# Optimization experiments

Hardware: AMD Instinct MI355X
Metric: run time of the kernel (lower is better)

Reference implementation:

```python
import jax, jax.numpy as jnp
import numpy as np

K_BUCKET = 144  # bucket size k from __init__


def setup_inputs() -> dict:
    key = jax.random.key(0)
    k1, k2 = jax.random.split(key)
    B, C, H, W = 8, 256, 96, 96
    A = 4                      # n_attentions (hash rounds)
    m = min((H * W) // 144, 128)  # = 64, per the source's m formula
    inputs = jax.random.normal(k1, (B, C, H, W), dtype=jnp.float32)
    random_matrices = jax.random.normal(k2, (A, C, m), dtype=jnp.float32)
    return {"inputs": inputs, "random_matrices": random_matrices}


def reference(inputs, random_matrices):
    B, C, H, W = inputs.shape
    A = random_matrices.shape[0]
    S = H * W
    k = K_BUCKET
    nb = S // k  # number of buckets

    # flatten(2,3).permute(0,2,1): [B, S, C]
    xf = inputs.reshape(B, C, S).transpose(0, 2, 1)

    # LSH random projection: [B, A, S, m]
    rot = jnp.einsum('bsc,acm->basm', xf, random_matrices)
    # max-hash over projection dim: [B, A, S]
    hash_code = jnp.max(rot, axis=-1)

    # descending sort -> permutation of sequence positions per (batch, round)
    idx = jnp.argsort(-hash_code, axis=2)            # [B, A, S] int

    # gather features into hash order: [B, A, S, C]
    xg = jnp.take_along_axis(xf[:, None, :, :], idx[..., None], axis=2)
    # split into buckets of size k: [B, A, nb, k, C]
    xb = xg.reshape(B, A, nb, k, C)

    # per-bucket self-attention (non-local attention restricted to bucket)
    scale = 1.0 / jnp.sqrt(jnp.asarray(C, dtype=xb.dtype))
    scores = jnp.einsum('banic,banjc->banij', xb, xb) * scale  # [B,A,nb,k,k]
    probs = jax.nn.softmax(scores, axis=-1)
    ob = jnp.einsum('banij,banjc->banic', probs, xb)           # [B,A,nb,k,C]

    # scatter bucket outputs back to original positions via inverse permutation
    out_sorted = ob.reshape(B, A, S, C)
    inv = jnp.argsort(idx, axis=2)                             # inverse permutation
    out = jnp.take_along_axis(out_sorted, inv[..., None], axis=2)  # [B,A,S,C]

    # average over hash rounds -> [B, S, C] (output layout matches torch.zeros(n,h*w,c))
    return jnp.mean(out, axis=1)
```

## Files before the change

kernel.cpp:

```cpp
#include <hip/hip_runtime.h>
#include <math.h>

#define B_ 8
#define C_ 256
#define S_ 9216
#define A_ 4
#define K_ 144
#define NB_ 64
#define SORTN 16384
#define XSS 261

typedef __bf16 bf16x8 __attribute__((ext_vector_type(8)));
typedef float f32x4 __attribute__((ext_vector_type(4)));
typedef double f64x4 __attribute__((ext_vector_type(4)));
#define MFMA(a, b, c) __builtin_amdgcn_mfma_f32_16x16x32_bf16(a, b, c, 0, 0, 0)
#define MFMA64(a, b, c) __builtin_amdgcn_mfma_f64_16x16x4f64(a, b, c, 0, 0, 0)

__device__ __forceinline__ unsigned short f2bf(float f) {
  unsigned int u = __float_as_uint(f);
  u = (u + 0x7FFFu + ((u >> 16) & 1u)) >> 16;
  return (unsigned short)u;
}
__device__ __forceinline__ float bf2f(unsigned short u) {
  return __uint_as_float(((unsigned int)u) << 16);
}

__global__ __launch_bounds__(256) void t_kernel(const float* __restrict__ in,
                                                unsigned short* __restrict__ xf16) {
  __shared__ float tile[32][33];
  int b = blockIdx.z;
  int c0 = blockIdx.y << 5, s0 = blockIdx.x << 5;
  int x = threadIdx.x & 31, y = threadIdx.x >> 5;
  const float* ip = in + ((size_t)b * C_ + c0 + y) * S_ + s0 + x;
#pragma unroll
  for (int k = 0; k < 32; k += 8) tile[y + k][x] = ip[(size_t)k * S_];
  __syncthreads();
  int xx = threadIdx.x & 15;
  int yy = threadIdx.x >> 4;
#pragma unroll
  for (int k = 0; k < 32; k += 16) {
    int s = s0 + yy + k;
    unsigned int* dst = (unsigned int*)(xf16 + ((size_t)b * S_ + s) * C_ + c0);
    dst[xx] = (unsigned int)f2bf(tile[2 * xx][yy + k]) |
              ((unsigned int)f2bf(tile[2 * xx + 1][yy + k]) << 16);
  }
}

__global__ __launch_bounds__(256) void cvt_r_kernel(const float* __restrict__ RM,
                                                    double* __restrict__ R64) {
  int i = blockIdx.x * 256 + threadIdx.x;
  if (i < A_ * C_ * 64) R64[i] = (double)RM[i];
}

__global__ __launch_bounds__(256, 2) void hash_kernel(const float* __restrict__ in,
                                                      const double* __restrict__ R64,
                                                      unsigned long long* __restrict__ keys) {
  __shared__ float Xs[64 * XSS];
  int blk = blockIdx.x;
  int chunk = blk % (S_ / 64);
  int b = blk / (S_ / 64);
  int s0 = chunk * 64;
  int tid = threadIdx.x;
  int a = __builtin_amdgcn_readfirstlane(tid >> 6);
  int lane = tid & 63, lr = lane & 15, lg = lane >> 4;

  for (int e = tid; e < C_ * 16; e += 256) {
    int c = e >> 4, sq = (e & 15) << 2;
    float4 v = *(const float4*)&in[((size_t)b * C_ + c) * S_ + s0 + sq];
    Xs[(sq + 0) * XSS + c] = v.x;
    Xs[(sq + 1) * XSS + c] = v.y;
    Xs[(sq + 2) * XSS + c] = v.z;
    Xs[(sq + 3) * XSS + c] = v.w;
  }
  __syncthreads();

  const double* __restrict__ Rb = R64 + (size_t)a * C_ * 64;
  f64x4 acc[4][4];
#pragma unroll
  for (int rt = 0; rt < 4; ++rt)
#pragma unroll
    for (int ct = 0; ct < 4; ++ct) acc[rt][ct] = (f64x4){0.0, 0.0, 0.0, 0.0};

#pragma unroll 2
  for (int k = 0; k < 64; ++k) {
    int c = k * 4 + lg;
    double bv[4], av[4];
#pragma unroll
    for (int ct = 0; ct < 4; ++ct) bv[ct] = Rb[(size_t)c * 64 + ct * 16 + lr];
#pragma unroll
    for (int rt = 0; rt < 4; ++rt) av[rt] = (double)Xs[(rt * 16 + lr) * XSS + c];
#pragma unroll
    for (int rt = 0; rt < 4; ++rt)
#pragma unroll
      for (int ct = 0; ct < 4; ++ct) acc[rt][ct] = MFMA64(av[rt], bv[ct], acc[rt][ct]);
  }

  unsigned long long* kb = keys + ((size_t)(b * A_ + a)) * SORTN;
#pragma unroll
  for (int rt = 0; rt < 4; ++rt) {
    double mj[4];
#pragma unroll
    for (int j = 0; j < 4; ++j) {
      double m0 = acc[rt][0][j] > acc[rt][1][j] ? acc[rt][0][j] : acc[rt][1][j];
      double m1 = acc[rt][2][j] > acc[rt][3][j] ? acc[rt][2][j] : acc[rt][3][j];
      mj[j] = m0 > m1 ? m0 : m1;
    }
#pragma unroll
    for (int off = 1; off < 16; off <<= 1)
#pragma unroll
      for (int j = 0; j < 4; ++j) {
        double o = __shfl_xor(mj[j], off);
        mj[j] = mj[j] > o ? mj[j] : o;
      }
    if (lr == 0) {
#pragma unroll
      for (int j = 0; j < 4; ++j) {
        int s = s0 + rt * 16 + lg * 4 + j;
        unsigned long long u = (unsigned long long)__double_as_longlong(mj[j]);
        unsigned long long mono = u ^ ((u >> 63) ? ~0ull : 0x8000000000000000ull);
        kb[s] = (~mono & ~0x3FFFull) | (unsigned long long)s;
      }
    }
  }
}

__global__ __launch_bounds__(256) void pad_kernel(unsigned long long* __restrict__ keys) {
  int e = blockIdx.x * 256 + threadIdx.x;
  int ba = e / (SORTN - S_), off = e % (SORTN - S_);
  keys[(size_t)ba * SORTN + S_ + off] = ~0ull;
}

__global__ __launch_bounds__(256) void sort_local_kernel(unsigned long long* __restrict__ keys) {
  __shared__ unsigned long long lk[2048];
  int blk = blockIdx.x;
  int ba = blk >> 3, chunk = blk & 7;
  size_t base = (size_t)ba * SORTN + (size_t)chunk * 2048;
  int posbase = chunk * 2048;
  int tid = threadIdx.x;
  for (int i = tid; i < 2048; i += 256) lk[i] = keys[base + i];
  for (int k = 2; k <= 2048; k <<= 1)
    for (int j = k >> 1; j > 0; j >>= 1) {
      __syncthreads();
      for (int i = tid; i < 2048; i += 256) {
        int l = i ^ j;
        if (l > i) {
          unsigned long long a = lk[i], b = lk[l];
          bool up = (((posbase + i) & k) == 0);
          bool sw = up ? (a > b) : (a < b);
          if (sw) { lk[i] = b; lk[l] = a; }
        }
      }
    }
  __syncthreads();
  for (int i = tid; i < 2048; i += 256) keys[base + i] = lk[i];
}

template <int CS>
__global__ __launch_bounds__(512) void sort_merge_kernel(unsigned long long* __restrict__ keys,
                                                         int k, int startj) {
  __shared__ unsigned long long lk[CS];
  int blk = blockIdx.x;
  const int nch = SORTN / CS;
  int ba = blk / nch, chunk = blk % nch;
  size_t base = (size_t)ba * SORTN + (size_t)chunk * CS;
  int posbase = chunk * CS;
  int tid = threadIdx.x;
  for (int i = tid; i < CS; i += 512) lk[i] = keys[base + i];
  for (int j = startj; j > 0; j >>= 1) {
    __syncthreads();
    for (int i = tid; i < CS; i += 512) {
      int l = i ^ j;
      if (l > i) {
        unsigned long long a = lk[i], b = lk[l];
        bool up = (((posbase + i) & k) == 0);
        bool sw = up ? (a > b) : (a < b);
        if (sw) { lk[i] = b; lk[l] = a; }
      }
    }
  }
  __syncthreads();
  for (int i = tid; i < CS; i += 512) keys[base + i] = lk[i];
}

__global__ __launch_bounds__(256) void sort_gpass_kernel(unsigned long long* __restrict__ keys) {
  int e = blockIdx.x * 256 + threadIdx.x;
  int ba = e >> 13, p = e & 8191;
  size_t base = (size_t)ba * SORTN;
  unsigned long long a = keys[base + p], b = keys[base + p + 8192];
  if (a > b) {
    keys[base + p] = b;
    keys[base + p + 8192] = a;
  }
}

__global__ __launch_bounds__(512) void sort_final_kernel(const unsigned long long* __restrict__ keys,
                                                         int* __restrict__ idxs,
                                                         int* __restrict__ invs) {
  __shared__ unsigned long long lk[8192];
  int blk = blockIdx.x;
  int ba = blk >> 1, chunk = blk & 1;
  size_t base = (size_t)ba * SORTN + (size_t)chunk * 8192;
  int posbase = chunk * 8192;
  int tid = threadIdx.x;
  for (int i = tid; i < 8192; i += 512) lk[i] = keys[base + i];
  for (int j = 4096; j > 0; j >>= 1) {
    __syncthreads();
    for (int i = tid; i < 8192; i += 512) {
      int l = i ^ j;
      if (l > i) {
        unsigned long long a = lk[i], b = lk[l];
        if (a > b) { lk[i] = b; lk[l] = a; }
      }
    }
  }
  __syncthreads();
  int* ob = idxs + (size_t)ba * S_;
  int* iv = invs + (size_t)ba * S_;
  for (int i = tid; i < 8192; i += 512) {
    int pos = posbase + i;
    if (pos < S_) {
      int orig = (int)(lk[i] & 0x3FFFull);
      ob[pos] = orig;
      iv[orig] = pos;
    }
  }
}

__global__ __launch_bounds__(512, 4) void attn_kernel(const unsigned short* __restrict__ xf16,
                                                      const float* __restrict__ in,
                                                      const int* __restrict__ idxs,
                                                      unsigned short* __restrict__ outacc,
                                                      float* __restrict__ out,
                                                      int use_xf, int path_a) {
  __shared__ __align__(16) unsigned short R1[K_ * 128];
  __shared__ __align__(16) unsigned short R2[128 * K_];
  __shared__ __align__(16) unsigned short Ps8[16 * 160];
  const int blk = blockIdx.x;
  const int r = blk & 63, a = (blk >> 6) & 3, b = blk >> 8;
  const int tid = threadIdx.x;
  const int w = __builtin_amdgcn_readfirstlane(tid >> 6);
  const int lane = tid & 63, lr = lane & 15, lg = lane >> 4;
  const int* __restrict__ idxr = idxs + ((size_t)(b * A_ + a)) * S_ + r * K_;
  const unsigned short* __restrict__ xfb = xf16 + (size_t)b * S_ * C_;
  const float scale = 0.0625f;

  auto stage = [&](int ch) {
    if (use_xf) {
      for (int e = tid; e < K_ * 16; e += 512) {
        int i = e >> 4, q8 = (e & 15) << 3;
        int s = idxr[i];
        uint4 d = *(const uint4*)(xfb + (size_t)s * C_ + ch * 128 + q8);
        *(uint4*)&R1[i * 128 + (q8 ^ ((i & 7) << 3))] = d;
      }
    } else {
      for (int e = tid; e < K_ * 128; e += 512) {
        int i = e >> 7, c = e & 127;
        R1[i * 128 + (c ^ ((i & 7) << 3))] =
            f2bf(in[((size_t)b * C_ + ch * 128 + c) * S_ + idxr[i]]);
      }
    }
  };

  auto transp = [&]() {
    int L = (tid & 7) | ((tid >> 8) << 3);
    int jb = (tid >> 3) & 31;
    if (jb < 18) {
      uint4 rv[8];
#pragma unroll
      for (int rr = 0; rr < 8; ++rr)
        rv[rr] = *(const uint4*)&R1[(jb * 8 + rr) * 128 + ((L * 8) ^ (rr << 3))];
#pragma unroll
      for (int cc = 0; cc < 8; ++cc) {
        unsigned int sel = (cc & 1) ? 0x07060302u : 0x05040100u;
        uint4 d;
        unsigned int* dd = (unsigned int*)&d;
#pragma unroll
        for (int q = 0; q < 4; ++q) {
          unsigned int lo = ((const unsigned int*)&rv[2 * q])[cc >> 1];
          unsigned int hi = ((const unsigned int*)&rv[2 * q + 1])[cc >> 1];
          dd[q] = __builtin_amdgcn_perm(hi, lo, sel);
        }
        *(uint4*)&R2[(L * 8 + cc) * K_ + jb * 8] = d;
      }
    }
  };

  for (int e = tid; e < 16 * 160 / 2; e += 512) ((unsigned int*)Ps8)[e] = 0u;
  stage(0);
  __syncthreads();

  f32x4 acc[9], acc8, acc8b;
#pragma unroll
  for (int jt = 0; jt < 9; ++jt) acc[jt] = (f32x4){0.f, 0.f, 0.f, 0.f};
  acc8 = (f32x4){0.f, 0.f, 0.f, 0.f};
  acc8b = (f32x4){0.f, 0.f, 0.f, 0.f};
  auto qk_half = [&]() {
    for (int kt = 0; kt < 4; ++kt) {
      int c0 = kt * 32 + lg * 8;
      int sw = c0 ^ ((lr & 7) << 3);
      bf16x8 fr[9];
#pragma unroll
      for (int jt = 0; jt < 9; ++jt)
        fr[jt] = *(const bf16x8*)&R1[(jt * 16 + lr) * 128 + sw];
      bf16x8 bT = *(const bf16x8*)&R1[(w * 16 + lr) * 128 + sw];
#pragma unroll
      for (int jt = 0; jt < 9; ++jt) acc[jt] = MFMA(fr[jt], bT, acc[jt]);
      acc8 = MFMA(bT, fr[8], acc8);
      if (w == 0) acc8b = MFMA(fr[8], fr[8], acc8b);
    }
  };
  qk_half();
  transp();
  __syncthreads();
  stage(1);
  __syncthreads();
  qk_half();

#pragma unroll
  for (int mm = 0; mm < 4; ++mm)
    Ps8[lr * 160 + (w * 16 + lg * 4 + mm)] = f2bf(acc8[mm]);
  if (w == 0) {
#pragma unroll
    for (int mm = 0; mm < 4; ++mm)
      Ps8[lr * 160 + (128 + lg * 4 + mm)] = f2bf(acc8b[mm]);
  }

  float mx = -1e30f;
#pragma unroll
  for (int jt = 0; jt < 9; ++jt)
#pragma unroll
    for (int mm = 0; mm < 4; ++mm) mx = fmaxf(mx, acc[jt][mm]);
  mx = fmaxf(mx, __shfl_xor(mx, 16));
  mx = fmaxf(mx, __shfl_xor(mx, 32));
  float sum = 0.f;
#pragma unroll
  for (int jt = 0; jt < 9; ++jt)
#pragma unroll
    for (int mm = 0; mm < 4; ++mm) {
      float e = __expf((acc[jt][mm] - mx) * scale);
      acc[jt][mm] = e;
      sum += e;
    }
  sum += __shfl_xor(sum, 16);
  sum += __shfl_xor(sum, 32);
  float inv = 1.0f / sum;
  unsigned int pk[18];
#pragma unroll
  for (int jt = 0; jt < 9; ++jt) {
    pk[2 * jt] = (unsigned int)f2bf(acc[jt][0] * inv) |
                 ((unsigned int)f2bf(acc[jt][1] * inv) << 16);
    pk[2 * jt + 1] = (unsigned int)f2bf(acc[jt][2] * inv) |
                     ((unsigned int)f2bf(acc[jt][3] * inv) << 16);
  }

  const int src1 = lr + 16 * ((2 * lg) & 3);
  const int src2 = lr + 16 * ((2 * lg + 1) & 3);
  const int hi8 = lg >> 1;
  bf16x8 pa[5];
#pragma unroll
  for (int kt = 0; kt < 5; ++kt) {
    const int jt0 = (kt < 4) ? 2 * kt : 7;
    unsigned int d0a = __shfl(pk[2 * jt0], src1), d0b = __shfl(pk[2 * jt0 + 2], src1);
    unsigned int d1a = __shfl(pk[2 * jt0 + 1], src1), d1b = __shfl(pk[2 * jt0 + 3], src1);
    unsigned int d2a = __shfl(pk[2 * jt0], src2), d2b = __shfl(pk[2 * jt0 + 2], src2);
    unsigned int d3a = __shfl(pk[2 * jt0 + 1], src2), d3b = __shfl(pk[2 * jt0 + 3], src2);
    uint4 d;
    d.x = hi8 ? d0b : d0a;
    d.y = hi8 ? d1b : d1a;
    d.z = hi8 ? d2b : d2a;
    d.w = hi8 ? d3b : d3a;
    if (kt == 4 && lg < 2) d = make_uint4(0u, 0u, 0u, 0u);
    pa[kt] = *(bf16x8*)&d;
  }
  __syncthreads();

  for (int rr = 0; rr < 2; ++rr) {
    int row = 2 * w + rr;
    float x0 = bf2f(Ps8[row * 160 + lane]);
    float x1 = bf2f(Ps8[row * 160 + 64 + lane]);
    float x2 = (lane < 16) ? bf2f(Ps8[row * 160 + 128 + lane]) : -1e30f;
    float m8 = fmaxf(fmaxf(x0, x1), x2);
    for (int off = 32; off; off >>= 1) m8 = fmaxf(m8, __shfl_xor(m8, off));
    float e0 = __expf((x0 - m8) * scale), e1 = __expf((x1 - m8) * scale);
    float e2 = (lane < 16) ? __expf((x2 - m8) * scale) : 0.f;
    float s8 = e0 + e1 + e2;
    for (int off = 32; off; off >>= 1) s8 += __shfl_xor(s8, off);
    float i8 = 1.0f / s8;
    Ps8[row * 160 + lane] = f2bf(e0 * i8);
    Ps8[row * 160 + 64 + lane] = f2bf(e1 * i8);
    if (lane < 16) Ps8[row * 160 + 128 + lane] = f2bf(e2 * i8);
  }
  __syncthreads();

  unsigned short* oaRow =
      path_a ? outacc + (((size_t)(b * A_ + a)) * S_ + (size_t)r * K_) * C_ : nullptr;
  auto pv_half = [&](int h) {
    f32x4 o[8], o8;
#pragma unroll
    for (int ct = 0; ct < 8; ++ct) o[ct] = (f32x4){0.f, 0.f, 0.f, 0.f};
    o8 = (f32x4){0.f, 0.f, 0.f, 0.f};
#pragma unroll
    for (int kt = 0; kt < 5; ++kt) {
      int J0 = (kt < 4) ? kt * 32 : 112;
      int j8 = (kt < 4) ? (J0 + lg * 8) : ((lg < 2) ? (144 + lg * 8) : (112 + lg * 8));
      bf16x8 pa8 = *(const bf16x8*)&Ps8[lr * 160 + j8];
#pragma unroll
      for (int ct = 0; ct < 8; ++ct) {
        bf16x8 vb = *(const bf16x8*)&R2[(ct * 16 + lr) * K_ + J0 + lg * 8];
        o[ct] = MFMA(pa[kt], vb, o[ct]);
        if (ct == w) o8 = MFMA(pa8, vb, o8);
      }
    }
    if (path_a) {
#pragma unroll
      for (int ct = 0; ct < 8; ++ct) {
        int cg = h * 128 + ct * 16 + lr;
#pragma unroll
        for (int rr = 0; rr < 4; ++rr) {
          int i = w * 16 + lg * 4 + rr;
          oaRow[(size_t)i * C_ + cg] = f2bf(o[ct][rr]);
        }
      }
      int cg8 = h * 128 + w * 16 + lr;
#pragma unroll
      for (int rr = 0; rr < 4; ++rr)
        oaRow[(size_t)(128 + lg * 4 + rr) * C_ + cg8] = f2bf(o8[rr]);
    } else {
#pragma unroll
      for (int ct = 0; ct < 8; ++ct) {
        int cg = h * 128 + ct * 16 + lr;
#pragma unroll
        for (int rr = 0; rr < 4; ++rr) {
          int s = idxr[w * 16 + lg * 4 + rr];
          atomicAdd(&out[((size_t)b * S_ + s) * C_ + cg], o[ct][rr] * 0.25f);
        }
      }
      int cg8 = h * 128 + w * 16 + lr;
#pragma unroll
      for (int rr = 0; rr < 4; ++rr) {
        int s = idxr[128 + lg * 4 + rr];
        atomicAdd(&out[((size_t)b * S_ + s) * C_ + cg8], o8[rr] * 0.25f);
      }
    }
  };

  pv_half(0);
  __syncthreads();
  transp();
  __syncthreads();
  pv_half(1);
}

__global__ __launch_bounds__(256) void reduce_kernel(const unsigned short* __restrict__ outacc,
                                                     const int* __restrict__ invs,
                                                     float* __restrict__ out) {
  size_t i = (size_t)blockIdx.x * 256 + threadIdx.x;
  size_t n4 = (size_t)B_ * S_ * C_ / 4;
  if (i >= n4) return;
  int cq = (int)(i & (C_ / 4 - 1));
  size_t bs = i >> 6;
  int s = (int)(bs % S_);
  int b = (int)(bs / S_);
  float4 sum = make_float4(0.f, 0.f, 0.f, 0.f);
#pragma unroll
  for (int a = 0; a < A_; ++a) {
    size_t base = (size_t)(b * A_ + a) * S_;
    int p = invs[base + s];
    ushort4 v = *(const ushort4*)(outacc + (base + p) * C_ + cq * 4);
    sum.x += bf2f(v.x);
    sum.y += bf2f(v.y);
    sum.z += bf2f(v.z);
    sum.w += bf2f(v.w);
  }
  float4 rv = make_float4(sum.x * 0.25f, sum.y * 0.25f, sum.z * 0.25f, sum.w * 0.25f);
  *(float4*)(out + ((size_t)b * S_ + s) * C_ + cq * 4) = rv;
}

__global__ __launch_bounds__(256) void zero_kernel(float* __restrict__ out) {
  size_t i = (size_t)blockIdx.x * 256 + threadIdx.x;
  size_t n4 = (size_t)B_ * S_ * C_ / 4;
  if (i >= n4) return;
  *(float4*)(out + i * 4) = make_float4(0.f, 0.f, 0.f, 0.f);
}

extern "C" void kernel_launch(void* const* d_in, const int* in_sizes, int n_in,
                              void* d_out, int out_size, void* d_ws, size_t ws_size,
                              hipStream_t stream) {
  const float* in = (const float*)d_in[0];
  const float* RM = (const float*)d_in[1];
  float* out = (float*)d_out;
  const size_t r64_b  = (size_t)A_ * C_ * 64 * 8;
  const size_t key_b  = (size_t)B_ * A_ * SORTN * 8;
  const size_t idx_b  = (size_t)B_ * A_ * S_ * 4;
  const size_t inv_b  = (size_t)B_ * A_ * S_ * 4;
  const size_t xf_b   = (size_t)B_ * S_ * C_ * 2;
  const size_t accw_b = (size_t)B_ * A_ * S_ * C_ * 2;
  char* ws = (char*)d_ws;
  size_t off = 0;
  double* R64 = (double*)(ws + off); off += r64_b;
  unsigned long long* keys = (unsigned long long*)(ws + off); off += key_b;
  int* idxs = (int*)(ws + off); off += idx_b;
  int* invs = (int*)(ws + off); off += inv_b;
  int use_xf = ws_size >= off + xf_b;
  unsigned short* xf16 = nullptr;
  if (use_xf) { xf16 = (unsigned short*)(ws + off); off += xf_b; }
  int path_a = ws_size >= off + accw_b;
  unsigned short* outacc = nullptr;
  if (path_a) { outacc = (unsigned short*)(ws + off); off += accw_b; }

  cvt_r_kernel<<<dim3((A_ * C_ * 64 + 255) / 256), 256, 0, stream>>>(RM, R64);
  if (use_xf)
    t_kernel<<<dim3(S_ / 32, C_ / 32, B_), 256, 0, stream>>>(in, xf16);
  hash_kernel<<<dim3(B_ * (S_ / 64)), 256, 0, stream>>>(in, R64, keys);
  pad_kernel<<<dim3(B_ * A_ * (SORTN - S_) / 256), 256, 0, stream>>>(keys);
  sort_local_kernel<<<dim3(B_ * A_ * 8), 256, 0, stream>>>(keys);
  sort_merge_kernel<4096><<<dim3(B_ * A_ * 4), 512, 0, stream>>>(keys, 4096, 2048);
  sort_merge_kernel<8192><<<dim3(B_ * A_ * 2), 512, 0, stream>>>(keys, 8192, 4096);
  sort_gpass_kernel<<<dim3(B_ * A_ * 8192 / 256), 256, 0, stream>>>(keys);
  sort_final_kernel<<<dim3(B_ * A_ * 2), 512, 0, stream>>>(keys, idxs, invs);

  size_t n4 = (size_t)B_ * S_ * C_ / 4;
  int rb = (int)((n4 + 255) / 256);
  if (!path_a) zero_kernel<<<dim3(rb), 256, 0, stream>>>(out);
  attn_kernel<<<dim3(B_ * A_ * NB_), 512, 0, stream>>>(xf16, in, idxs, outacc, out, use_xf, path_a);
  if (path_a) reduce_kernel<<<dim3(rb), 256, 0, stream>>>(outacc, invs, out);
}
```

Baseline: 495.0 us.

## Compute LSH hash with split-bf16 MFMA and refine top candidates in fp64

Replaces the fp64 MFMA projection in the hash kernel with a three-term hi/lo split-bf16 MFMA approximation. For each position it keeps the projections within a small threshold of the max and recomputes only those candidates exactly in fp64 to produce the sort key. R is pre-packed into hi/lo bf16 fragments in the conversion kernel. This aims to cut the cost of slow fp64 MFMA throughput. The risk is a wrong key when more than four candidates fall near the max or the approximation error exceeds the threshold.

```diff
diff --git a/kernel.cpp b/kernel.cpp
--- a/kernel.cpp
+++ b/kernel.cpp
@@ -12,9 +12,7 @@
 
 typedef __bf16 bf16x8 __attribute__((ext_vector_type(8)));
 typedef float f32x4 __attribute__((ext_vector_type(4)));
-typedef double f64x4 __attribute__((ext_vector_type(4)));
 #define MFMA(a, b, c) __builtin_amdgcn_mfma_f32_16x16x32_bf16(a, b, c, 0, 0, 0)
-#define MFMA64(a, b, c) __builtin_amdgcn_mfma_f64_16x16x4f64(a, b, c, 0, 0, 0)
 
 __device__ __forceinline__ unsigned short f2bf(float f) {
   unsigned int u = __float_as_uint(f);
@@ -47,15 +45,30 @@
 }
 
 __global__ __launch_bounds__(256) void cvt_r_kernel(const float* __restrict__ RM,
-                                                    double* __restrict__ R64) {
+                                                    double* __restrict__ R64,
+                                                    unsigned short* __restrict__ rpkhi,
+                                                    unsigned short* __restrict__ rpklo) {
   int i = blockIdx.x * 256 + threadIdx.x;
-  if (i < A_ * C_ * 64) R64[i] = (double)RM[i];
+  if (i >= A_ * C_ * 64) return;
+  R64[i] = (double)RM[i];
+  int q = i & 7, lane = (i >> 3) & 63, mt = (i >> 9) & 3, kc = (i >> 11) & 7, a = i >> 14;
+  int c = kc * 32 + (lane >> 4) * 8 + q;
+  int m = mt * 16 + (lane & 15);
+  float r = RM[(a * C_ + c) * 64 + m];
+  unsigned short hi = f2bf(r);
+  unsigned short lo = f2bf(r - bf2f(hi));
+  rpkhi[i] = hi;
+  rpklo[i] = lo;
 }
 
 __global__ __launch_bounds__(256, 2) void hash_kernel(const float* __restrict__ in,
                                                       const double* __restrict__ R64,
+                                                      const unsigned short* __restrict__ rpkhi,
+                                                      const unsigned short* __restrict__ rpklo,
                                                       unsigned long long* __restrict__ keys) {
   __shared__ float Xs[64 * XSS];
+  __shared__ int cnt[A_ * 64];
+  __shared__ short cand[A_ * 64 * 4];
   int blk = blockIdx.x;
   int chunk = blk % (S_ / 64);
   int b = blk / (S_ / 64);
@@ -64,6 +77,7 @@
   int a = __builtin_amdgcn_readfirstlane(tid >> 6);
   int lane = tid & 63, lr = lane & 15, lg = lane >> 4;
 
+  for (int e = tid; e < A_ * 64; e += 256) cnt[e] = 0;
   for (int e = tid; e < C_ * 16; e += 256) {
     int c = e >> 4, sq = (e & 15) << 2;
     float4 v = *(const float4*)&in[((size_t)b * C_ + c) * S_ + s0 + sq];
@@ -74,54 +88,103 @@
   }
   __syncthreads();
 
-  const double* __restrict__ Rb = R64 + (size_t)a * C_ * 64;
-  f64x4 acc[4][4];
-#pragma unroll
-  for (int rt = 0; rt < 4; ++rt)
-#pragma unroll
-    for (int ct = 0; ct < 4; ++ct) acc[rt][ct] = (f64x4){0.0, 0.0, 0.0, 0.0};
-
+  f32x4 acc[4][4];
+#pragma unroll
+  for (int st = 0; st < 4; ++st)
+#pragma unroll
+    for (int mt = 0; mt < 4; ++mt) acc[st][mt] = (f32x4){0.f, 0.f, 0.f, 0.f};
+
+  for (int kc = 0; kc < 8; ++kc) {
+    bf16x8 ahi[4], alo[4];
+#pragma unroll
+    for (int st = 0; st < 4; ++st) {
+      ushort hs[8], ls[8];
+#pragma unroll
+      for (int q = 0; q < 8; ++q) {
+        float xv = Xs[(st * 16 + lr) * XSS + kc * 32 + lg * 8 + q];
+        hs[q] = f2bf(xv);
+        ls[q] = f2bf(xv - bf2f(hs[q]));
+      }
+      uint4 hu, lu;
+      hu.x = hs[0] | ((unsigned)hs[1] << 16); hu.y = hs[2] | ((unsigned)hs[3] << 16);
+      hu.z = hs[4] | ((unsigned)hs[5] << 16); hu.w = hs[6] | ((unsigned)hs[7] << 16);
+      lu.x = ls[0] | ((unsigned)ls[1] << 16); lu.y = ls[2] | ((unsigned)ls[3] << 16);
+      lu.z = ls[4] | ((unsigned)ls[5] << 16); lu.w = ls[6] | ((unsigned)ls[7] << 16);
+      ahi[st] = *(bf16x8*)&hu;
+      alo[st] = *(bf16x8*)&lu;
+    }
+    bf16x8 bh[4], bl[4];
+#pragma unroll
+    for (int mt = 0; mt < 4; ++mt) {
+      size_t off = (size_t)(((a * 8 + kc) * 4 + mt) * 64 + lane) * 8;
+      uint4 hv = *(const uint4*)(rpkhi + off);
+      uint4 lv = *(const uint4*)(rpklo + off);
+      bh[mt] = *(bf16x8*)&hv;
+      bl[mt] = *(bf16x8*)&lv;
+    }
+#pragma unroll
+    for (int st = 0; st < 4; ++st)
+#pragma unroll
+      for (int mt = 0; mt < 4; ++mt) {
+        acc[st][mt] = MFMA(ahi[st], bh[mt], acc[st][mt]);
+        acc[st][mt] = MFMA(ahi[st], bl[mt], acc[st][mt]);
+        acc[st][mt] = MFMA(alo[st], bh[mt], acc[st][mt]);
+      }
+  }
+
+  const float thr = 1.5e-2f;
+#pragma unroll
+  for (int st = 0; st < 4; ++st) {
+    f32x4 vmax;
+#pragma unroll
+    for (int reg = 0; reg < 4; ++reg) {
+      float m0 = fmaxf(acc[st][0][reg], acc[st][1][reg]);
+      float m1 = fmaxf(acc[st][2][reg], acc[st][3][reg]);
+      vmax[reg] = fmaxf(m0, m1);
+    }
+#pragma unroll
+    for (int off = 1; off < 16; off <<= 1)
+#pragma unroll
+      for (int reg = 0; reg < 4; ++reg)
+        vmax[reg] = fmaxf(vmax[reg], __shfl_xor(vmax[reg], off));
+#pragma unroll
+    for (int reg = 0; reg < 4; ++reg) {
+      int s = st * 16 + lg * 4 + reg;
+      float cut = vmax[reg] - thr;
+#pragma unroll
+      for (int mt = 0; mt < 4; ++mt) {
+        if (acc[st][mt][reg] >= cut) {
+          int slot = atomicAdd(&cnt[a * 64 + s], 1);
+          if (slot < 4) cand[(a * 64 + s) * 4 + slot] = (short)(mt * 16 + lr);
+        }
+      }
+    }
+  }
+  __syncthreads();
+
+  int s = lane;
+  int n = cnt[a * 64 + s];
+  n = n > 4 ? 4 : n;
+  const double* __restrict__ Ra = R64 + (size_t)a * C_ * 64;
+  double best = -1e300;
+  for (int t = 0; t < n; ++t) {
+    int m = cand[(a * 64 + s) * 4 + t];
+    const double* __restrict__ Rm = Ra + m;
+    double d0 = 0, d1 = 0, d2 = 0, d3 = 0;
 #pragma unroll 2
-  for (int k = 0; k < 64; ++k) {
-    int c = k * 4 + lg;
-    double bv[4], av[4];
-#pragma unroll
-    for (int ct = 0; ct < 4; ++ct) bv[ct] = Rb[(size_t)c * 64 + ct * 16 + lr];
-#pragma unroll
-    for (int rt = 0; rt < 4; ++rt) av[rt] = (double)Xs[(rt * 16 + lr) * XSS + c];
-#pragma unroll
-    for (int rt = 0; rt < 4; ++rt)
-#pragma unroll
-      for (int ct = 0; ct < 4; ++ct) acc[rt][ct] = MFMA64(av[rt], bv[ct], acc[rt][ct]);
-  }
-
-  unsigned long long* kb = keys + ((size_t)(b * A_ + a)) * SORTN;
-#pragma unroll
-  for (int rt = 0; rt < 4; ++rt) {
-    double mj[4];
-#pragma unroll
-    for (int j = 0; j < 4; ++j) {
-      double m0 = acc[rt][0][j] > acc[rt][1][j] ? acc[rt][0][j] : acc[rt][1][j];
-      double m1 = acc[rt][2][j] > acc[rt][3][j] ? acc[rt][2][j] : acc[rt][3][j];
-      mj[j] = m0 > m1 ? m0 : m1;
-    }
-#pragma unroll
-    for (int off = 1; off < 16; off <<= 1)
-#pragma unroll
-      for (int j = 0; j < 4; ++j) {
-        double o = __shfl_xor(mj[j], off);
-        mj[j] = mj[j] > o ? mj[j] : o;
-      }
-    if (lr == 0) {
-#pragma unroll
-      for (int j = 0; j < 4; ++j) {
-        int s = s0 + rt * 16 + lg * 4 + j;
-        unsigned long long u = (unsigned long long)__double_as_longlong(mj[j]);
-        unsigned long long mono = u ^ ((u >> 63) ? ~0ull : 0x8000000000000000ull);
-        kb[s] = (~mono & ~0x3FFFull) | (unsigned long long)s;
-      }
-    }
-  }
+    for (int c = 0; c < C_; c += 4) {
+      d0 = fma((double)Xs[s * XSS + c + 0], Rm[(size_t)(c + 0) * 64], d0);
+      d1 = fma((double)Xs[s * XSS + c + 1], Rm[(size_t)(c + 1) * 64], d1);
+      d2 = fma((double)Xs[s * XSS + c + 2], Rm[(size_t)(c + 2) * 64], d2);
+      d3 = fma((double)Xs[s * XSS + c + 3], Rm[(size_t)(c + 3) * 64], d3);
+    }
+    double d = (d0 + d1) + (d2 + d3);
+    best = best > d ? best : d;
+  }
+  unsigned long long u = (unsigned long long)__double_as_longlong(best);
+  unsigned long long mono = u ^ ((u >> 63) ? ~0ull : 0x8000000000000000ull);
+  keys[((size_t)(b * A_ + a)) * SORTN + s0 + s] =
+      (~mono & ~0x3FFFull) | (unsigned long long)(s0 + s);
 }
 
 __global__ __launch_bounds__(256) void pad_kernel(unsigned long long* __restrict__ keys) {
@@ -490,6 +553,7 @@
   const float* RM = (const float*)d_in[1];
   float* out = (float*)d_out;
   const size_t r64_b  = (size_t)A_ * C_ * 64 * 8;
+  const size_t rpk_b  = (size_t)A_ * C_ * 64 * 2;
   const size_t key_b  = (size_t)B_ * A_ * SORTN * 8;
   const size_t idx_b  = (size_t)B_ * A_ * S_ * 4;
   const size_t inv_b  = (size_t)B_ * A_ * S_ * 4;
@@ -498,6 +562,8 @@
   char* ws = (char*)d_ws;
   size_t off = 0;
   double* R64 = (double*)(ws + off); off += r64_b;
+  unsigned short* rpkhi = (unsigned short*)(ws + off); off += rpk_b;
+  unsigned short* rpklo = (unsigned short*)(ws + off); off += rpk_b;
   unsigned long long* keys = (unsigned long long*)(ws + off); off += key_b;
   int* idxs = (int*)(ws + off); off += idx_b;
   int* invs = (int*)(ws + off); off += inv_b;
@@ -508,10 +574,10 @@
   unsigned short* outacc = nullptr;
   if (path_a) { outacc = (unsigned short*)(ws + off); off += accw_b; }
 
-  cvt_r_kernel<<<dim3((A_ * C_ * 64 + 255) / 256), 256, 0, stream>>>(RM, R64);
+  cvt_r_kernel<<<dim3((A_ * C_ * 64 + 255) / 256), 256, 0, stream>>>(RM, R64, rpkhi, rpklo);
   if (use_xf)
     t_kernel<<<dim3(S_ / 32, C_ / 32, B_), 256, 0, stream>>>(in, xf16);
-  hash_kernel<<<dim3(B_ * (S_ / 64)), 256, 0, stream>>>(in, R64, keys);
+  hash_kernel<<<dim3(B_ * (S_ / 64)), 256, 0, stream>>>(in, R64, rpkhi, rpklo, keys);
   pad_kernel<<<dim3(B_ * A_ * (SORTN - S_) / 256), 256, 0, stream>>>(keys);
   sort_local_kernel<<<dim3(B_ * A_ * 8), 256, 0, stream>>>(keys);
   sort_merge_kernel<4096><<<dim3(B_ * A_ * 4), 512, 0, stream>>>(keys, 4096, 2048);
```

Result: faster. 429.3 us (-13.3%).
